# Kernel tuning notes

Hardware: AMD Instinct MI355X
Metric: run time of the kernel (lower is better)

Reference implementation:

```python
import jax, jax.numpy as jnp
import numpy as np

EPS = 1e-12  # torch F.normalize eps

def _cam(fmap, w):
    # torch: sum over C of w[1,C,R,1,1] * fmap[B,C,1,H,W] -> (B,R,H,W)
    # expressed as an efficient contraction (1x1 conv / GEMM)
    return jnp.einsum('bchw,rc->brhw', fmap, w)

def _embedding(fmap, w, b):
    pooled = fmap.mean(axis=(-2, -1))           # (B,C) AdaptiveAvgPool2d(1)
    return pooled @ w.T + b                      # (B,R)

def _certainty(cam):
    B, R = cam.shape[:2]
    flat = cam.reshape(B, R, -1)
    return jnp.std(flat, axis=-1, ddof=1)        # torch .std() is unbiased

def _avgpool_to(x, out_hw):
    # adaptive avg pool with integer ratio == reshape-mean
    B, R, H, W = x.shape
    oh, ow = out_hw
    return x.reshape(B, R, oh, H // oh, ow, W // ow).mean(axis=(3, 5))

def _link(low_cam, high_cam):
    low_cam = jax.lax.stop_gradient(low_cam)
    high_cam = jax.lax.stop_gradient(high_cam)
    if low_cam.shape[2:] != high_cam.shape[2:]:
        low_cam = _avgpool_to(low_cam, high_cam.shape[2:])
    B = low_cam.shape[0]
    lo = low_cam.reshape(B, low_cam.shape[1], -1)
    hi = high_cam.reshape(B, high_cam.shape[1], -1)
    lo = lo / jnp.maximum(jnp.linalg.norm(lo, axis=-1, keepdims=True), EPS)
    hi = hi / jnp.maximum(jnp.linalg.norm(hi, axis=-1, keepdims=True), EPS)
    return jnp.einsum('bmi,bni->mn', lo, hi) / B

def setup_inputs() -> dict:
    key = jax.random.key(0)
    ks = jax.random.split(key, 6)
    B, R = 64, 128
    chans = [512, 1024, 2048]
    hws = [28, 14, 7]
    inp = {}
    for l in range(3):
        inp[f'fmap{l}'] = jax.random.normal(ks[l], (B, chans[l], hws[l], hws[l]), dtype=jnp.float32)
        inp[f'w{l}'] = jax.random.normal(ks[3 + l], (R, chans[l]), dtype=jnp.float32) * 0.02
        inp[f'b{l}'] = jnp.zeros((R,), dtype=jnp.float32)
    return inp

def reference(fmap0, fmap1, fmap2, w0, b0, w1, b1, w2, b2):
    fmaps = [fmap0, fmap1, fmap2]
    ws = [w0, w1, w2]
    bs = [b0, b1, b2]
    embeddings = [_embedding(f, w, b) for f, w, b in zip(fmaps, ws, bs)]
    cams = [_cam(f, w) for f, w in zip(fmaps, ws)]
    certainties = [_certainty(c) for c in cams]
    links = [_link(cams[l - 1], cams[l]) for l in range(1, 3)]
    return (*embeddings, *certainties, *links)
```

## Files before the change

### kernel.cpp

```cpp
#include <hip/hip_runtime.h>
#include <stdint.h>

#define R 128
#define NB 64

#define CAM0_OFF 0
#define CAM1_OFF 6422528
#define CAM2_OFF 8028160
#define POOL0_OFF 8429568
#define POOL1_OFF 10035200
#define WB_OFF    10436608
#define PART_OFF  10665984
#define NORM_OFF  12763136

typedef __bf16 bf16;
typedef bf16 v2bf __attribute__((ext_vector_type(2)));
typedef bf16 v8bf __attribute__((ext_vector_type(8)));
typedef float f4v __attribute__((ext_vector_type(4)));

#define ASM_BARRIER() asm volatile("s_waitcnt lgkmcnt(0)\n\ts_barrier" ::: "memory")

__global__ void prep_w(const float* __restrict__ w0, const float* __restrict__ w1,
                       const float* __restrict__ w2, bf16* __restrict__ wb) {
    int id = blockIdx.x * 256 + threadIdx.x;
    float v;
    if (id < 65536)       v = w0[id];
    else if (id < 196608) v = w1[id - 65536];
    else                  v = w2[id - 196608];
    wb[id] = (bf16)v;
}

__global__ __launch_bounds__(256) void cam_gemm(
    const float* __restrict__ f0, const float* __restrict__ f1,
    const float* __restrict__ f2, const bf16* __restrict__ wb,
    float* __restrict__ ws) {
    __shared__ bf16 ldsB[64 * 72];

    int bid = blockIdx.x, tid = threadIdx.x;
    int lvl, b, i0;
    if (bid < 64)       { lvl = 2; b = bid; i0 = 0; }
    else if (bid < 320) { int t = bid - 64; lvl = 1; b = t >> 2;
                          int ti = t & 3; i0 = ti < 3 ? ti * 64 : 132; }
    else                { int t = bid - 320; lvl = 0; b = t / 13;
                          int ti = t - b * 13; i0 = ti < 12 ? ti * 64 : 720; }
    const int C  = (lvl == 0) ? 512 : (lvl == 1) ? 1024 : 2048;
    const int HW = (lvl == 0) ? 784 : (lvl == 1) ? 196  : 49;
    const float* fmap = (lvl == 0) ? f0 : (lvl == 1) ? f1 : f2;
    const bf16*  wbl  = wb + ((lvl == 0) ? 0 : (lvl == 1) ? 65536 : 196608);
    float* cam = ws + ((lvl == 0) ? CAM0_OFF : (lvl == 1) ? CAM1_OFF : CAM2_OFF);

    int ku2[2], i4u[2], gbase[2], ldsd[2][4];
#pragma unroll
    for (int un = 0; un < 2; ++un) {
        int u = un * 256 + tid;
        int d = u >> 4;
        ku2[un] = d * 2;
        int g = u & 15; i4u[un] = g * 4;
        gbase[un] = b * C * HW + ku2[un] * HW + i0 + i4u[un];
#pragma unroll
        for (int e = 0; e < 4; ++e) {
            int i = i4u[un] + e;
            int grp = (d >> 2) ^ ((i >> 3) & 7);
            ldsd[un][e] = i * 72 + grp * 8 + (d & 3) * 2;
        }
    }
    const int lane = tid & 63, wave = tid >> 6;
    const int lm = lane & 15, q = lane >> 4;
    const int wm = (wave >> 1) * 64, wn = (wave & 1) * 32;
    int irow[2], ixor[2];
#pragma unroll
    for (int sn = 0; sn < 2; ++sn) {
        irow[sn] = wn + sn * 16 + lm;
        ixor[sn] = (irow[sn] >> 3) & 7;
    }
    const bf16* arow[4];
#pragma unroll
    for (int sm = 0; sm < 4; ++sm)
        arow[sm] = wbl + (wm + sm * 16 + lm) * C + q * 8;

    auto load_tile = [&](int kc, float4 (&r)[2][2]) {
        if (HW != 49) {
#pragma unroll
            for (int un = 0; un < 2; ++un) {
                const float* p = fmap + gbase[un] + kc * HW;
                r[un][0] = *(const float4*)p;
                r[un][1] = *(const float4*)(p + HW);
            }
        } else {
#pragma unroll
            for (int un = 0; un < 2; ++un) {
                const float* p = fmap + b * C * 49 + (kc + ku2[un]) * 49;
                int i4 = i4u[un];
                r[un][0].x = p[min(i4 + 0, 48)]; r[un][0].y = p[min(i4 + 1, 48)];
                r[un][0].z = p[min(i4 + 2, 48)]; r[un][0].w = p[min(i4 + 3, 48)];
                r[un][1].x = p[49 + min(i4 + 0, 48)]; r[un][1].y = p[49 + min(i4 + 1, 48)];
                r[un][1].z = p[49 + min(i4 + 2, 48)]; r[un][1].w = p[49 + min(i4 + 3, 48)];
            }
        }
    };

    f4v acc[4][2] = {};
    float4 pr[2][2];
    load_tile(0, pr);
    for (int kc = 0; kc < C; kc += 64) {
#pragma unroll
        for (int un = 0; un < 2; ++un) {
            v2bf t0 = { (bf16)pr[un][0].x, (bf16)pr[un][1].x };
            v2bf t1 = { (bf16)pr[un][0].y, (bf16)pr[un][1].y };
            v2bf t2 = { (bf16)pr[un][0].z, (bf16)pr[un][1].z };
            v2bf t3 = { (bf16)pr[un][0].w, (bf16)pr[un][1].w };
            *(v2bf*)&ldsB[ldsd[un][0]] = t0;
            *(v2bf*)&ldsB[ldsd[un][1]] = t1;
            *(v2bf*)&ldsB[ldsd[un][2]] = t2;
            *(v2bf*)&ldsB[ldsd[un][3]] = t3;
        }
        ASM_BARRIER();
        if (kc + 64 < C) load_tile(kc + 64, pr);
#pragma unroll
        for (int ks = 0; ks < 64; ks += 32) {
            v8bf af[4];
#pragma unroll
            for (int sm = 0; sm < 4; ++sm)
                af[sm] = *(const v8bf*)(arow[sm] + kc + ks);
            v8bf bfr[2];
#pragma unroll
            for (int sn = 0; sn < 2; ++sn) {
                int grp = (q + ((ks >> 5) << 2)) ^ ixor[sn];
                bfr[sn] = *(const v8bf*)&ldsB[irow[sn] * 72 + grp * 8];
            }
#pragma unroll
            for (int sm = 0; sm < 4; ++sm)
#pragma unroll
                for (int sn = 0; sn < 2; ++sn)
                    acc[sm][sn] = __builtin_amdgcn_mfma_f32_16x16x32_bf16(
                        af[sm], bfr[sn], acc[sm][sn], 0, 0, 0);
        }
        ASM_BARRIER();
    }
#pragma unroll
    for (int sn = 0; sn < 2; ++sn) {
        int i_n = i0 + irow[sn];
        if (i_n < HW) {
            int base = (b * R) * HW + i_n;
#pragma unroll
            for (int sm = 0; sm < 4; ++sm) {
#pragma unroll
                for (int reg = 0; reg < 4; ++reg) {
                    int r = wm + sm * 16 + q * 4 + reg;
                    cam[base + r * HW] = acc[sm][sn][reg];
                }
            }
        }
    }
}

__global__ __launch_bounds__(256) void post_k(
    float* __restrict__ ws, const float* __restrict__ b0,
    const float* __restrict__ b1, const float* __restrict__ b2,
    float* __restrict__ out) {
    __shared__ float plds[4 * 784];
    int gw = blockIdx.x * 4 + (threadIdx.x >> 6);
    int lane = threadIdx.x & 63;
    float* myl = plds + (threadIdx.x >> 6) * 784;
    int lvl = gw >> 13, row = gw & 8191;
    const int HW = (lvl == 0) ? 784 : (lvl == 1) ? 196 : 49;
    const float* cam = ws + ((lvl == 0) ? CAM0_OFF : (lvl == 1) ? CAM1_OFF : CAM2_OFF)
                        + (long)row * HW;
    float s = 0.f, ss = 0.f;
    for (int j = lane; j < HW; j += 64) {
        float v = cam[j]; s += v; ss += v * v; myl[j] = v;
    }
#pragma unroll
    for (int o = 32; o; o >>= 1) { s += __shfl_xor(s, o); ss += __shfl_xor(ss, o); }
    if (lane == 0) {
        const float* bias = (lvl == 0) ? b0 : (lvl == 1) ? b1 : b2;
        float mean = s / (float)HW;
        out[lvl * 8192 + row] = mean + bias[row & 127];
        float var = fmaxf(ss - s * mean, 0.f) / (float)(HW - 1);
        out[24576 + lvl * 8192 + row] = sqrtf(var);
        if (lvl >= 1)
            ws[NORM_OFF + (lvl - 1) * 8192 + row] = 1.0f / fmaxf(sqrtf(ss), 1e-12f);
    }
    if (lvl <= 1) {
        const int OP = (lvl == 0) ? 196 : 49;
        const int OW = (lvl == 0) ? 14 : 7;
        const int IW = (lvl == 0) ? 28 : 14;
        float vals[4]; float ssp = 0.f; int cnt = 0;
        for (int p = lane; p < OP; p += 64) {
            int oh = p / OW, ow = p - oh * OW;
            int i0 = oh * 2 * IW + ow * 2;
            float v = (myl[i0] + myl[i0 + 1] + myl[i0 + IW] + myl[i0 + IW + 1]) * 0.25f;
            vals[cnt++] = v; ssp += v * v;
        }
#pragma unroll
        for (int o = 32; o; o >>= 1) ssp += __shfl_xor(ssp, o);
        float inv = 1.0f / fmaxf(sqrtf(ssp), 1e-12f);
        float* dst = ws + ((lvl == 0) ? POOL0_OFF : POOL1_OFF) + (long)row * OP;
        cnt = 0;
        for (int p = lane; p < OP; p += 64) dst[p] = vals[cnt++] * inv;
    }
}

__device__ inline v8bf load_frag8(const float* __restrict__ row, int k0, int K) {
    v8bf f;
    if (k0 + 8 <= K && (K & 3) == 0) {
        float4 a = *(const float4*)(row + k0);
        float4 c = *(const float4*)(row + k0 + 4);
        f[0] = (bf16)a.x; f[1] = (bf16)a.y; f[2] = (bf16)a.z; f[3] = (bf16)a.w;
        f[4] = (bf16)c.x; f[5] = (bf16)c.y; f[6] = (bf16)c.z; f[7] = (bf16)c.w;
    } else {
#pragma unroll
        for (int j = 0; j < 8; ++j)
            f[j] = (k0 + j < K) ? (bf16)row[k0 + j] : (bf16)0.f;
    }
    return f;
}

__global__ __launch_bounds__(256) void link_mfma_k(const float* __restrict__ ws,
                                                   float* __restrict__ part) {
    int bid = blockIdx.x, tid = threadIdx.x;
    int lk = bid >> 6, b = bid & 63;
    const int K = lk ? 49 : 196;
    const float* lo = ws + (lk ? POOL1_OFF : POOL0_OFF) + (long)b * 128 * K;
    const float* hi = ws + (lk ? CAM2_OFF : CAM1_OFF) + (long)b * 128 * K;
    const float* nrmp = ws + NORM_OFF + lk * 8192 + b * 128;
    int lane = tid & 63, wv = tid >> 6;
    int lm = lane & 15, q = lane >> 4;
    int wm = (wv >> 1) * 64, wn = (wv & 1) * 64;
    f4v acc[4][4] = {};
    for (int kc = 0; kc < K; kc += 32) {
        v8bf af[4], bff[4];
#pragma unroll
        for (int sm = 0; sm < 4; ++sm)
            af[sm] = load_frag8(lo + (long)(wm + sm * 16 + lm) * K, kc + q * 8, K);
#pragma unroll
        for (int sn = 0; sn < 4; ++sn)
            bff[sn] = load_frag8(hi + (long)(wn + sn * 16 + lm) * K, kc + q * 8, K);
#pragma unroll
        for (int sm = 0; sm < 4; ++sm)
#pragma unroll
            for (int sn = 0; sn < 4; ++sn)
                acc[sm][sn] = __builtin_amdgcn_mfma_f32_16x16x32_bf16(
                    af[sm], bff[sn], acc[sm][sn], 0, 0, 0);
    }
    float* dstb = part + lk * 1048576 + b * 16384;
#pragma unroll
    for (int sn = 0; sn < 4; ++sn) {
        int n = wn + sn * 16 + lm;
        float sh = nrmp[n];
#pragma unroll
        for (int sm = 0; sm < 4; ++sm) {
#pragma unroll
            for (int reg = 0; reg < 4; ++reg) {
                int m = wm + sm * 16 + q * 4 + reg;
                dstb[m * 128 + n] = acc[sm][sn][reg] * sh;
            }
        }
    }
}

__global__ void linkred_k(const float* __restrict__ part, float* __restrict__ out) {
    int id = blockIdx.x * 256 + threadIdx.x;
    int lk = id >> 14, mn = id & 16383;
    const float* p = part + lk * 1048576 + mn;
    float s = 0.f;
#pragma unroll 8
    for (int b = 0; b < 64; ++b) s += p[b * 16384];
    out[49152 + lk * 16384 + mn] = s * (1.0f / 64.0f);
}

extern "C" void kernel_launch(void* const* d_in, const int* in_sizes, int n_in,
                              void* d_out, int out_size, void* d_ws, size_t ws_size,
                              hipStream_t stream) {
    const float* f0 = (const float*)d_in[0];
    const float* w0 = (const float*)d_in[1];
    const float* b0 = (const float*)d_in[2];
    const float* f1 = (const float*)d_in[3];
    const float* w1 = (const float*)d_in[4];
    const float* b1 = (const float*)d_in[5];
    const float* f2 = (const float*)d_in[6];
    const float* w2 = (const float*)d_in[7];
    const float* b2 = (const float*)d_in[8];
    float* ws = (float*)d_ws;
    float* out = (float*)d_out;
    bf16* wb = (bf16*)(ws + WB_OFF);

    prep_w<<<1792, 256, 0, stream>>>(w0, w1, w2, wb);
    cam_gemm<<<1152, 256, 0, stream>>>(f0, f1, f2, wb, ws);
    post_k<<<6144, 256, 0, stream>>>(ws, b0, b1, b2, out);
    link_mfma_k<<<128, 256, 0, stream>>>(ws, ws + PART_OFF);
    linkred_k<<<128, 256, 0, stream>>>(ws + PART_OFF, out);
}
```

Measured before the change: 330.8 us.

## Double-buffer CAM GEMM with 512-thread blocks; split link GEMM, transpose partials

The CAM GEMM moves to 512 threads per block. Each wave now covers a 32x32 output tile, and the LDS staging buffer becomes two ping-pong buffers so global loads for the next two K-chunks overlap compute. The link GEMM launches twice as many blocks, each handling half of the M rows. It writes partials with batch as the innermost dimension, so the reduction kernel reads 64 contiguous floats with float4 loads instead of strided accesses. The cost is more LDS per block, scattered strided stores in the link kernel, and smaller per-wave tiles that reuse A fragments less.

```diff
diff --git a/kernel.cpp b/kernel.cpp
--- a/kernel.cpp
+++ b/kernel.cpp
@@ -30,11 +30,11 @@
     wb[id] = (bf16)v;
 }
 
-__global__ __launch_bounds__(256) void cam_gemm(
+__global__ __launch_bounds__(512) void cam_gemm(
     const float* __restrict__ f0, const float* __restrict__ f1,
     const float* __restrict__ f2, const bf16* __restrict__ wb,
     float* __restrict__ ws) {
-    __shared__ bf16 ldsB[64 * 72];
+    __shared__ bf16 ldsB[2][64 * 72];
 
     int bid = blockIdx.x, tid = threadIdx.x;
     int lvl, b, i0;
@@ -49,93 +49,93 @@
     const bf16*  wbl  = wb + ((lvl == 0) ? 0 : (lvl == 1) ? 65536 : 196608);
     float* cam = ws + ((lvl == 0) ? CAM0_OFF : (lvl == 1) ? CAM1_OFF : CAM2_OFF);
 
-    int ku2[2], i4u[2], gbase[2], ldsd[2][4];
-#pragma unroll
-    for (int un = 0; un < 2; ++un) {
-        int u = un * 256 + tid;
-        int d = u >> 4;
-        ku2[un] = d * 2;
-        int g = u & 15; i4u[un] = g * 4;
-        gbase[un] = b * C * HW + ku2[un] * HW + i0 + i4u[un];
-#pragma unroll
-        for (int e = 0; e < 4; ++e) {
-            int i = i4u[un] + e;
-            int grp = (d >> 2) ^ ((i >> 3) & 7);
-            ldsd[un][e] = i * 72 + grp * 8 + (d & 3) * 2;
-        }
+    int d = tid >> 4;
+    int ku2 = d * 2;
+    int i4 = (tid & 15) * 4;
+    int gbase = b * C * HW + ku2 * HW + i0 + i4;
+    int ldsd[4];
+    int i4c[4];
+#pragma unroll
+    for (int e = 0; e < 4; ++e) {
+        int i = i4 + e;
+        int grp = (d >> 2) ^ ((i >> 3) & 7);
+        ldsd[e] = i * 72 + grp * 8 + (d & 3) * 2;
+        i4c[e] = min(i, 48);
     }
     const int lane = tid & 63, wave = tid >> 6;
     const int lm = lane & 15, q = lane >> 4;
-    const int wm = (wave >> 1) * 64, wn = (wave & 1) * 32;
+    const int wm = (wave >> 1) * 32, wn = (wave & 1) * 32;
     int irow[2], ixor[2];
 #pragma unroll
     for (int sn = 0; sn < 2; ++sn) {
         irow[sn] = wn + sn * 16 + lm;
         ixor[sn] = (irow[sn] >> 3) & 7;
     }
-    const bf16* arow[4];
-#pragma unroll
-    for (int sm = 0; sm < 4; ++sm)
+    const bf16* arow[2];
+#pragma unroll
+    for (int sm = 0; sm < 2; ++sm)
         arow[sm] = wbl + (wm + sm * 16 + lm) * C + q * 8;
 
-    auto load_tile = [&](int kc, float4 (&r)[2][2]) {
+    auto loadT = [&](int kc, float4 (&r)[2]) {
         if (HW != 49) {
-#pragma unroll
-            for (int un = 0; un < 2; ++un) {
-                const float* p = fmap + gbase[un] + kc * HW;
-                r[un][0] = *(const float4*)p;
-                r[un][1] = *(const float4*)(p + HW);
-            }
+            const float* p = fmap + gbase + kc * HW;
+            r[0] = *(const float4*)p;
+            r[1] = *(const float4*)(p + HW);
         } else {
-#pragma unroll
-            for (int un = 0; un < 2; ++un) {
-                const float* p = fmap + b * C * 49 + (kc + ku2[un]) * 49;
-                int i4 = i4u[un];
-                r[un][0].x = p[min(i4 + 0, 48)]; r[un][0].y = p[min(i4 + 1, 48)];
-                r[un][0].z = p[min(i4 + 2, 48)]; r[un][0].w = p[min(i4 + 3, 48)];
-                r[un][1].x = p[49 + min(i4 + 0, 48)]; r[un][1].y = p[49 + min(i4 + 1, 48)];
-                r[un][1].z = p[49 + min(i4 + 2, 48)]; r[un][1].w = p[49 + min(i4 + 3, 48)];
-            }
+            const float* p = fmap + b * C * 49 + (kc + ku2) * 49;
+            r[0].x = p[i4c[0]]; r[0].y = p[i4c[1]];
+            r[0].z = p[i4c[2]]; r[0].w = p[i4c[3]];
+            r[1].x = p[49 + i4c[0]]; r[1].y = p[49 + i4c[1]];
+            r[1].z = p[49 + i4c[2]]; r[1].w = p[49 + i4c[3]];
         }
     };
-
-    f4v acc[4][2] = {};
-    float4 pr[2][2];
-    load_tile(0, pr);
-    for (int kc = 0; kc < C; kc += 64) {
-#pragma unroll
-        for (int un = 0; un < 2; ++un) {
-            v2bf t0 = { (bf16)pr[un][0].x, (bf16)pr[un][1].x };
-            v2bf t1 = { (bf16)pr[un][0].y, (bf16)pr[un][1].y };
-            v2bf t2 = { (bf16)pr[un][0].z, (bf16)pr[un][1].z };
-            v2bf t3 = { (bf16)pr[un][0].w, (bf16)pr[un][1].w };
-            *(v2bf*)&ldsB[ldsd[un][0]] = t0;
-            *(v2bf*)&ldsB[ldsd[un][1]] = t1;
-            *(v2bf*)&ldsB[ldsd[un][2]] = t2;
-            *(v2bf*)&ldsB[ldsd[un][3]] = t3;
-        }
-        ASM_BARRIER();
-        if (kc + 64 < C) load_tile(kc + 64, pr);
+    auto stage = [&](float4 (&r)[2], bf16* buf) {
+        v2bf t0 = { (bf16)r[0].x, (bf16)r[1].x };
+        v2bf t1 = { (bf16)r[0].y, (bf16)r[1].y };
+        v2bf t2 = { (bf16)r[0].z, (bf16)r[1].z };
+        v2bf t3 = { (bf16)r[0].w, (bf16)r[1].w };
+        *(v2bf*)&buf[ldsd[0]] = t0;
+        *(v2bf*)&buf[ldsd[1]] = t1;
+        *(v2bf*)&buf[ldsd[2]] = t2;
+        *(v2bf*)&buf[ldsd[3]] = t3;
+    };
+
+    f4v acc[2][2] = {};
+    auto comp = [&](int kc, const bf16* buf) {
 #pragma unroll
         for (int ks = 0; ks < 64; ks += 32) {
-            v8bf af[4];
-#pragma unroll
-            for (int sm = 0; sm < 4; ++sm)
+            v8bf af[2];
+#pragma unroll
+            for (int sm = 0; sm < 2; ++sm)
                 af[sm] = *(const v8bf*)(arow[sm] + kc + ks);
             v8bf bfr[2];
 #pragma unroll
             for (int sn = 0; sn < 2; ++sn) {
                 int grp = (q + ((ks >> 5) << 2)) ^ ixor[sn];
-                bfr[sn] = *(const v8bf*)&ldsB[irow[sn] * 72 + grp * 8];
+                bfr[sn] = *(const v8bf*)&buf[irow[sn] * 72 + grp * 8];
             }
 #pragma unroll
-            for (int sm = 0; sm < 4; ++sm)
+            for (int sm = 0; sm < 2; ++sm)
 #pragma unroll
                 for (int sn = 0; sn < 2; ++sn)
                     acc[sm][sn] = __builtin_amdgcn_mfma_f32_16x16x32_bf16(
                         af[sm], bfr[sn], acc[sm][sn], 0, 0, 0);
         }
+    };
+
+    const int nIter = C >> 6;
+    float4 rA[2], rB[2];
+    loadT(0, rA);
+    loadT(64, rB);
+    for (int t = 0; t < nIter; t += 2) {
+        stage(rA, ldsB[0]);
         ASM_BARRIER();
+        if (t + 2 < nIter) loadT((t + 2) << 6, rA);
+        comp(t << 6, ldsB[0]);
+        stage(rB, ldsB[1]);
+        ASM_BARRIER();
+        if (t + 3 < nIter) loadT((t + 3) << 6, rB);
+        comp((t + 1) << 6, ldsB[1]);
     }
 #pragma unroll
     for (int sn = 0; sn < 2; ++sn) {
@@ -143,7 +143,7 @@
         if (i_n < HW) {
             int base = (b * R) * HW + i_n;
 #pragma unroll
-            for (int sm = 0; sm < 4; ++sm) {
+            for (int sm = 0; sm < 2; ++sm) {
 #pragma unroll
                 for (int reg = 0; reg < 4; ++reg) {
                     int r = wm + sm * 16 + q * 4 + reg;
@@ -219,41 +219,41 @@
 __global__ __launch_bounds__(256) void link_mfma_k(const float* __restrict__ ws,
                                                    float* __restrict__ part) {
     int bid = blockIdx.x, tid = threadIdx.x;
-    int lk = bid >> 6, b = bid & 63;
+    int lk = bid >> 7, rem = bid & 127;
+    int b = rem >> 1, mh = rem & 1;
     const int K = lk ? 49 : 196;
-    const float* lo = ws + (lk ? POOL1_OFF : POOL0_OFF) + (long)b * 128 * K;
+    const float* lo = ws + (lk ? POOL1_OFF : POOL0_OFF) + (long)(b * 128 + mh * 64) * K;
     const float* hi = ws + (lk ? CAM2_OFF : CAM1_OFF) + (long)b * 128 * K;
     const float* nrmp = ws + NORM_OFF + lk * 8192 + b * 128;
     int lane = tid & 63, wv = tid >> 6;
     int lm = lane & 15, q = lane >> 4;
-    int wm = (wv >> 1) * 64, wn = (wv & 1) * 64;
-    f4v acc[4][4] = {};
+    int wm = (wv >> 1) * 32, wn = (wv & 1) * 64;
+    f4v acc[2][4] = {};
     for (int kc = 0; kc < K; kc += 32) {
-        v8bf af[4], bff[4];
-#pragma unroll
-        for (int sm = 0; sm < 4; ++sm)
+        v8bf af[2], bff[4];
+#pragma unroll
+        for (int sm = 0; sm < 2; ++sm)
             af[sm] = load_frag8(lo + (long)(wm + sm * 16 + lm) * K, kc + q * 8, K);
 #pragma unroll
         for (int sn = 0; sn < 4; ++sn)
             bff[sn] = load_frag8(hi + (long)(wn + sn * 16 + lm) * K, kc + q * 8, K);
 #pragma unroll
-        for (int sm = 0; sm < 4; ++sm)
+        for (int sm = 0; sm < 2; ++sm)
 #pragma unroll
             for (int sn = 0; sn < 4; ++sn)
                 acc[sm][sn] = __builtin_amdgcn_mfma_f32_16x16x32_bf16(
                     af[sm], bff[sn], acc[sm][sn], 0, 0, 0);
     }
-    float* dstb = part + lk * 1048576 + b * 16384;
 #pragma unroll
     for (int sn = 0; sn < 4; ++sn) {
         int n = wn + sn * 16 + lm;
         float sh = nrmp[n];
 #pragma unroll
-        for (int sm = 0; sm < 4; ++sm) {
+        for (int sm = 0; sm < 2; ++sm) {
 #pragma unroll
             for (int reg = 0; reg < 4; ++reg) {
-                int m = wm + sm * 16 + q * 4 + reg;
-                dstb[m * 128 + n] = acc[sm][sn][reg] * sh;
+                int m = mh * 64 + wm + sm * 16 + q * 4 + reg;
+                part[(long)(lk * 16384 + m * 128 + n) * 64 + b] = acc[sm][sn][reg] * sh;
             }
         }
     }
@@ -261,12 +261,14 @@
 
 __global__ void linkred_k(const float* __restrict__ part, float* __restrict__ out) {
     int id = blockIdx.x * 256 + threadIdx.x;
-    int lk = id >> 14, mn = id & 16383;
-    const float* p = part + lk * 1048576 + mn;
+    const float* p = part + (long)id * 64;
     float s = 0.f;
-#pragma unroll 8
-    for (int b = 0; b < 64; ++b) s += p[b * 16384];
-    out[49152 + lk * 16384 + mn] = s * (1.0f / 64.0f);
+#pragma unroll
+    for (int j = 0; j < 16; ++j) {
+        float4 v = *(const float4*)(p + j * 4);
+        s += v.x + v.y + v.z + v.w;
+    }
+    out[49152 + id] = s * (1.0f / 64.0f);
 }
 
 extern "C" void kernel_launch(void* const* d_in, const int* in_sizes, int n_in,
@@ -286,8 +288,8 @@
     bf16* wb = (bf16*)(ws + WB_OFF);
 
     prep_w<<<1792, 256, 0, stream>>>(w0, w1, w2, wb);
-    cam_gemm<<<1152, 256, 0, stream>>>(f0, f1, f2, wb, ws);
+    cam_gemm<<<1152, 512, 0, stream>>>(f0, f1, f2, wb, ws);
     post_k<<<6144, 256, 0, stream>>>(ws, b0, b1, b2, out);
-    link_mfma_k<<<128, 256, 0, stream>>>(ws, ws + PART_OFF);
+    link_mfma_k<<<256, 256, 0, stream>>>(ws, ws + PART_OFF);
     linkred_k<<<128, 256, 0, stream>>>(ws + PART_OFF, out);
 }
```

New measurement: 308.8 us. 6.7% less time.
